# Performance work log

Measured on AMD Instinct MI355X. Metric: run time of the kernel, lower is better.

Reference implementation:

```python
import jax, jax.numpy as jnp
import numpy as np

D = 1024        # input_dim
H = 4096        # hidden_dim (expert FFN width)
RH = H // 2     # router hidden
E = 8           # expert_count
TOP_K = 2
N = 4096        # tokens
LN_EPS = 1e-5


def setup_inputs() -> dict:
    key = jax.random.key(0)
    ks = jax.random.split(key, 12)
    s_d = 1.0 / np.sqrt(D)
    s_h = 1.0 / np.sqrt(H)
    s_rh = 1.0 / np.sqrt(RH)
    return {
        "x": jax.random.normal(ks[0], (N, D), jnp.float32),
        "ln_g": jnp.ones((D,), jnp.float32),
        "ln_b": jnp.zeros((D,), jnp.float32),
        # router: Linear(D, RH) -> ReLU -> Linear(RH, E)
        "rw1": jax.random.uniform(ks[1], (D, RH), jnp.float32, -s_d, s_d),
        "rb1": jax.random.uniform(ks[2], (RH,), jnp.float32, -s_d, s_d),
        "rw2": jax.random.uniform(ks[3], (RH, E), jnp.float32, -s_rh, s_rh),
        "rb2": jax.random.uniform(ks[4], (E,), jnp.float32, -s_rh, s_rh),
        # experts: E x (Linear(D, H) -> ReLU -> Linear(H, D)); dropout is identity in eval
        "ew1": jax.random.uniform(ks[5], (E, D, H), jnp.float32, -s_d, s_d),
        "eb1": jax.random.uniform(ks[6], (E, H), jnp.float32, -s_d, s_d),
        "ew2": jax.random.uniform(ks[7], (E, H, D), jnp.float32, -s_h, s_h),
        "eb2": jax.random.uniform(ks[8], (E, D), jnp.float32, -s_h, s_h),
    }


def reference(x, ln_g, ln_b, rw1, rb1, rw2, rb2, ew1, eb1, ew2, eb2):
    residual = x
    # LayerNorm
    mu = jnp.mean(x, axis=-1, keepdims=True)
    var = jnp.mean(jnp.square(x - mu), axis=-1, keepdims=True)
    xn = (x - mu) * jax.lax.rsqrt(var + LN_EPS) * ln_g + ln_b
    # Router MLP + softmax + top-k with renormalized gates
    logits = jax.nn.relu(xn @ rw1 + rb1) @ rw2 + rb2          # [N, E]
    probs = jax.nn.softmax(logits, axis=-1)
    vals, idx = jax.lax.top_k(probs, TOP_K)                    # [N, K]
    vals = vals / jnp.sum(vals, axis=-1, keepdims=True)
    # combine weights per expert: [N, E]
    combine = jnp.sum(jax.nn.one_hot(idx, E, dtype=vals.dtype) * vals[..., None], axis=1)
    # dense grouped expert FFN: h [E, N, H], y [E, N, D]
    h = jax.nn.relu(jnp.einsum("nd,edh->enh", xn, ew1) + eb1[:, None, :])
    y = jnp.einsum("enh,ehd->end", h, ew2) + eb2[:, None, :]
    out = residual + jnp.einsum("end,ne->nd", y, combine)
    return out
```

## Files before the change

### kernel.cpp

```cpp
#include <hip/hip_runtime.h>
#include <stdint.h>

#define D_    1024
#define H_    4096
#define RH_   2048
#define E_    8
#define N_    4096
#define NK_   8192
#define MT_MAX 71
#define DELTA_MARGIN 1e-4f
#define FIX_CAP 256

typedef __bf16 bf16x8 __attribute__((ext_vector_type(8)));
typedef float  f32x4  __attribute__((ext_vector_type(4)));


__device__ __forceinline__ unsigned short f2bf(float f) {
  union { float f; unsigned u; } v; v.f = f;
  unsigned r = v.u + 0x7fffu + ((v.u >> 16) & 1u);
  return (unsigned short)(r >> 16);
}
__device__ __forceinline__ float bf2f(unsigned short h) {
  union { unsigned u; float f; } v; v.u = ((unsigned)h) << 16;
  return v.f;
}

#define GLOAD16(gp, lp) \
  __builtin_amdgcn_global_load_lds((__attribute__((address_space(1))) void*)(void*)(gp), \
                                   (__attribute__((address_space(3))) void*)(lp), 16, 0, 0)

__global__ __launch_bounds__(256) void k_transpose(const float* __restrict__ in,
                                                   unsigned short* __restrict__ outH,
                                                   unsigned short* __restrict__ outL,
                                                   int R, int C) {
  __shared__ float t[32][33];
  const int b = blockIdx.z;
  const int c0 = blockIdx.x * 32, r0 = blockIdx.y * 32;
  const int lx = threadIdx.x & 31, ly = threadIdx.x >> 5;
  const long inB = (long)R * C;
  #pragma unroll
  for (int i = 0; i < 4; i++) {
    int r = r0 + ly + i * 8;
    t[ly + i * 8][lx] = in[b * inB + (long)r * C + c0 + lx];
  }
  __syncthreads();
  #pragma unroll
  for (int i = 0; i < 4; i++) {
    int c = c0 + ly + i * 8;
    float v = t[lx][ly + i * 8];
    unsigned short h = f2bf(v);
    long oi = b * inB + (long)c * R + r0 + lx;
    outH[oi] = h;
    if (outL) outL[oi] = f2bf(v - bf2f(h));
  }
}

__global__ __launch_bounds__(256) void k_layernorm(const float* __restrict__ x,
                                                   const float* __restrict__ g,
                                                   const float* __restrict__ b,
                                                   unsigned short* __restrict__ xnh,
                                                   unsigned short* __restrict__ xnl) {
  __shared__ float red[4];
  const int n = blockIdx.x, tid = threadIdx.x;
  float4 v = ((const float4*)(x + (long)n * D_))[tid];
  float s = v.x + v.y + v.z + v.w;
  #pragma unroll
  for (int o = 32; o >= 1; o >>= 1) s += __shfl_xor(s, o, 64);
  if ((tid & 63) == 0) red[tid >> 6] = s;
  __syncthreads();
  float mean = (red[0] + red[1] + red[2] + red[3]) * (1.f / D_);
  __syncthreads();
  float d0 = v.x - mean, d1 = v.y - mean, d2 = v.z - mean, d3 = v.w - mean;
  float ss = d0 * d0 + d1 * d1 + d2 * d2 + d3 * d3;
  #pragma unroll
  for (int o = 32; o >= 1; o >>= 1) ss += __shfl_xor(ss, o, 64);
  if ((tid & 63) == 0) red[tid >> 6] = ss;
  __syncthreads();
  float rstd = rsqrtf((red[0] + red[1] + red[2] + red[3]) * (1.f / D_) + 1e-5f);
  float4 gg = ((const float4*)g)[tid];
  float4 bb = ((const float4*)b)[tid];
  float xn0 = d0 * rstd * gg.x + bb.x;
  float xn1 = d1 * rstd * gg.y + bb.y;
  float xn2 = d2 * rstd * gg.z + bb.z;
  float xn3 = d3 * rstd * gg.w + bb.w;
  unsigned short h0 = f2bf(xn0), h1 = f2bf(xn1), h2 = f2bf(xn2), h3 = f2bf(xn3);
  ((ushort4*)xnh)[(long)n * 256 + tid] = make_ushort4(h0, h1, h2, h3);
  ((ushort4*)xnl)[(long)n * 256 + tid] = make_ushort4(
      f2bf(xn0 - bf2f(h0)), f2bf(xn1 - bf2f(h1)),
      f2bf(xn2 - bf2f(h2)), f2bf(xn3 - bf2f(h3)));
}

__global__ void k_init(int* ctl) { if (threadIdx.x < 36) ctl[threadIdx.x] = 0; }

__global__ __launch_bounds__(256) void k_router_gemm(const unsigned short* __restrict__ xh,
                                                     const unsigned short* __restrict__ xl,
                                                     const unsigned short* __restrict__ bhT,
                                                     const unsigned short* __restrict__ blT,
                                                     const float* __restrict__ rb1,
                                                     float* __restrict__ h_r) {
  __shared__ __align__(16) unsigned short Ah[128 * 32], Al[128 * 32], Bh[128 * 32], Bl[128 * 32];
  const int tid = threadIdx.x, lane = tid & 63, wid = tid >> 6;
  const int m0 = blockIdx.x * 128, n0 = blockIdx.y * 128;
  const int wm = wid >> 1, wn = wid & 1;
  const int seg0 = wid * 2;
  const int srow = lane >> 2;
  const int scol = (lane & 3) * 8;
  const long a0 = (long)(m0 + seg0 * 16 + srow) * D_ + scol;
  const long a1 = a0 + 16 * D_;
  const long b0 = (long)(n0 + seg0 * 16 + srow) * D_ + scol;
  const long b1 = b0 + 16 * D_;
  const int rl = lane & 15, kh8 = (lane >> 4) * 8;
  f32x4 acc[4][4];
  #pragma unroll
  for (int i = 0; i < 4; i++)
    #pragma unroll
    for (int j = 0; j < 4; j++) acc[i][j] = 0.f;

  for (int k0 = 0; k0 < D_; k0 += 32) {
    GLOAD16(xh + a0 + k0, Ah + seg0 * 512);
    GLOAD16(xh + a1 + k0, Ah + seg0 * 512 + 512);
    GLOAD16(xl + a0 + k0, Al + seg0 * 512);
    GLOAD16(xl + a1 + k0, Al + seg0 * 512 + 512);
    GLOAD16(bhT + b0 + k0, Bh + seg0 * 512);
    GLOAD16(bhT + b1 + k0, Bh + seg0 * 512 + 512);
    GLOAD16(blT + b0 + k0, Bl + seg0 * 512);
    GLOAD16(blT + b1 + k0, Bl + seg0 * 512 + 512);
    __syncthreads();
    bf16x8 bhf[4], blf[4];
    #pragma unroll
    for (int ni = 0; ni < 4; ni++) {
      int r = (wn * 64 + ni * 16 + rl) * 32 + kh8;
      bhf[ni] = *(const bf16x8*)(Bh + r);
      blf[ni] = *(const bf16x8*)(Bl + r);
    }
    #pragma unroll
    for (int mi = 0; mi < 4; mi++) {
      int r = (wm * 64 + mi * 16 + rl) * 32 + kh8;
      bf16x8 ah = *(const bf16x8*)(Ah + r);
      bf16x8 al = *(const bf16x8*)(Al + r);
      #pragma unroll
      for (int ni = 0; ni < 4; ni++) {
        acc[mi][ni] = __builtin_amdgcn_mfma_f32_16x16x32_bf16(ah, bhf[ni], acc[mi][ni], 0, 0, 0);
        acc[mi][ni] = __builtin_amdgcn_mfma_f32_16x16x32_bf16(ah, blf[ni], acc[mi][ni], 0, 0, 0);
        acc[mi][ni] = __builtin_amdgcn_mfma_f32_16x16x32_bf16(al, bhf[ni], acc[mi][ni], 0, 0, 0);
      }
    }
    __syncthreads();
  }
  const int rg4 = (lane >> 4) * 4;
  #pragma unroll
  for (int ni = 0; ni < 4; ni++) {
    int col = n0 + wn * 64 + ni * 16 + rl;
    float bias = rb1[col];
    #pragma unroll
    for (int mi = 0; mi < 4; mi++) {
      int row = m0 + wm * 64 + mi * 16 + rg4;
      #pragma unroll
      for (int r = 0; r < 4; r++) {
        float v = acc[mi][ni][r] + bias;
        h_r[(long)(row + r) * RH_ + col] = v > 0.f ? v : 0.f;
      }
    }
  }
}

__global__ __launch_bounds__(256) void k_logits_top2(const float* __restrict__ h_r,
                                                     const float* __restrict__ rw2,
                                                     const float* __restrict__ rb2,
                                                     int* __restrict__ sel, float* __restrict__ gate,
                                                     int* __restrict__ marked, int* __restrict__ mcount) {
  const int lane = threadIdx.x & 63, wid = threadIdx.x >> 6;
  const int n = blockIdx.x * 4 + wid;
  float p[8] = {0, 0, 0, 0, 0, 0, 0, 0};
  const float* hr = h_r + (long)n * RH_;
  for (int i = 0; i < RH_ / 64; i++) {
    int c = i * 64 + lane;
    float v = hr[c];
    float4 wa = ((const float4*)(rw2 + c * 8))[0];
    float4 wb = ((const float4*)(rw2 + c * 8))[1];
    p[0] += v * wa.x; p[1] += v * wa.y; p[2] += v * wa.z; p[3] += v * wa.w;
    p[4] += v * wb.x; p[5] += v * wb.y; p[6] += v * wb.z; p[7] += v * wb.w;
  }
  #pragma unroll
  for (int e = 0; e < 8; e++)
    #pragma unroll
    for (int s = 32; s >= 1; s >>= 1) p[e] += __shfl_xor(p[e], s, 64);
  if (lane == 0) {
    float l1 = -1e30f, l2 = -1e30f, l3 = -1e30f; int e1 = 0, e2 = 0;
    #pragma unroll
    for (int e = 0; e < 8; e++) {
      float v = p[e] + rb2[e];
      if (v > l1)      { l3 = l2; l2 = l1; e2 = e1; l1 = v; e1 = e; }
      else if (v > l2) { l3 = l2; l2 = v; e2 = e; }
      else if (v > l3) { l3 = v; }
    }
    float g1 = 1.f / (1.f + expf(l2 - l1));
    sel[n * 2] = e1; sel[n * 2 + 1] = e2;
    gate[n * 2] = g1; gate[n * 2 + 1] = 1.f - g1;
    if (l2 - l3 < DELTA_MARGIN) { int i = atomicAdd(mcount, 1); marked[i] = n; }
  }
}

__global__ __launch_bounds__(256) void k_fixup1(const float* __restrict__ x,
                                                const float* __restrict__ ln_g, const float* __restrict__ ln_b,
                                                const float* __restrict__ rw1, const float* __restrict__ rb1,
                                                const int* __restrict__ marked, const int* __restrict__ mcount,
                                                double* __restrict__ hsbuf) {
  __shared__ float xs[D_];
  __shared__ float redf[4];
  __shared__ double part[64][5];
  const int tid = threadIdx.x;
  int cnt = *mcount; if (cnt > FIX_CAP) cnt = FIX_CAP;
  const int blkTok = blockIdx.x >> 5;
  const int chunk  = blockIdx.x & 31;
  for (int mi = blkTok; mi < cnt; mi += FIX_CAP) {
    const int n = marked[mi];
    float4 v = ((const float4*)(x + (long)n * D_))[tid];
    float s = v.x + v.y + v.z + v.w;
    #pragma unroll
    for (int o = 32; o >= 1; o >>= 1) s += __shfl_xor(s, o, 64);
    if ((tid & 63) == 0) redf[tid >> 6] = s;
    __syncthreads();
    float mean = (redf[0] + redf[1] + redf[2] + redf[3]) * (1.f / D_);
    __syncthreads();
    float d0 = v.x - mean, d1 = v.y - mean, d2 = v.z - mean, d3 = v.w - mean;
    float ss = d0 * d0 + d1 * d1 + d2 * d2 + d3 * d3;
    #pragma unroll
    for (int o = 32; o >= 1; o >>= 1) ss += __shfl_xor(ss, o, 64);
    if ((tid & 63) == 0) redf[tid >> 6] = ss;
    __syncthreads();
    float rstd = rsqrtf((redf[0] + redf[1] + redf[2] + redf[3]) * (1.f / D_) + 1e-5f);
    float4 gg = ((const float4*)ln_g)[tid];
    float4 bb = ((const float4*)ln_b)[tid];
    xs[tid * 4 + 0] = d0 * rstd * gg.x + bb.x;
    xs[tid * 4 + 1] = d1 * rstd * gg.y + bb.y;
    xs[tid * 4 + 2] = d2 * rstd * gg.z + bb.z;
    xs[tid * 4 + 3] = d3 * rstd * gg.w + bb.w;
    __syncthreads();
    const int lcol = tid & 63, prt = tid >> 6;
    const int col = chunk * 64 + lcol;
    const float* rp = rw1 + (long)(prt * 256) * RH_ + col;
    const float* xp = xs + prt * 256;
    double a0 = 0, a1 = 0, a2 = 0, a3 = 0;
    #pragma unroll 4
    for (int d = 0; d < 256; d += 4) {
      float w0 = rp[(long)(d + 0) * RH_];
      float w1 = rp[(long)(d + 1) * RH_];
      float w2 = rp[(long)(d + 2) * RH_];
      float w3 = rp[(long)(d + 3) * RH_];
      a0 += (double)xp[d + 0] * (double)w0;
      a1 += (double)xp[d + 1] * (double)w1;
      a2 += (double)xp[d + 2] * (double)w2;
      a3 += (double)xp[d + 3] * (double)w3;
    }
    part[lcol][prt] = (a0 + a1) + (a2 + a3);
    __syncthreads();
    if (tid < 64) {
      double a = (part[tid][0] + part[tid][1]) + (part[tid][2] + part[tid][3])
               + (double)rb1[chunk * 64 + tid];
      hsbuf[(long)mi * RH_ + chunk * 64 + tid] = a > 0.0 ? a : 0.0;
    }
    __syncthreads();
  }
}

__global__ __launch_bounds__(256) void k_fixup2(const double* __restrict__ hsbuf,
                                                const float* __restrict__ rw2, const float* __restrict__ rb2,
                                                const int* __restrict__ marked, const int* __restrict__ mcount,
                                                int* __restrict__ sel, float* __restrict__ gate) {
  __shared__ double red2[256];
  const int tid = threadIdx.x;
  int cnt = *mcount; if (cnt > FIX_CAP) cnt = FIX_CAP;
  for (int mi = blockIdx.x; mi < cnt; mi += gridDim.x) {
    const int n = marked[mi];
    const double* hs = hsbuf + (long)mi * RH_;
    const int e = tid & 7, ch = tid >> 3;
    double pp = 0.0;
    for (int c = ch * 64; c < ch * 64 + 64; c++) pp += hs[c] * (double)rw2[c * 8 + e];
    red2[tid] = pp;
    __syncthreads();
    if (tid < 128) red2[tid] += red2[tid + 128];
    __syncthreads();
    if (tid < 64) red2[tid] += red2[tid + 64];
    __syncthreads();
    if (tid < 32) red2[tid] += red2[tid + 32];
    __syncthreads();
    if (tid < 16) red2[tid] += red2[tid + 16];
    __syncthreads();
    if (tid < 8) red2[tid] += red2[tid + 8];
    __syncthreads();
    if (tid == 0) {
      double l1 = -1e300, l2 = -1e300; int e1 = 0, e2 = 0;
      for (int ee = 0; ee < 8; ee++) {
        double vv = red2[ee] + (double)rb2[ee];
        if (vv > l1)      { l2 = l1; e2 = e1; l1 = vv; e1 = ee; }
        else if (vv > l2) { l2 = vv; e2 = ee; }
      }
      double g1 = 1.0 / (1.0 + exp(l2 - l1));
      sel[n * 2] = e1; sel[n * 2 + 1] = e2;
      gate[n * 2] = (float)g1; gate[n * 2 + 1] = (float)(1.0 - g1);
    }
    __syncthreads();
  }
}

__global__ void k_count(const int* __restrict__ sel, int* ctl) {
  int n = blockIdx.x * 256 + threadIdx.x;
  if (n >= N_) return;
  atomicAdd(&ctl[sel[n * 2]], 1);
  atomicAdd(&ctl[sel[n * 2 + 1]], 1);
}
__global__ void k_offsets(int* ctl) {
  if (threadIdx.x == 0 && blockIdx.x == 0) {
    int t = 0, tt = 0;
    for (int e = 0; e < 8; e++) {
      ctl[8 + e] = t; ctl[17 + e] = tt; ctl[26 + e] = t;
      t += ctl[e]; tt += (ctl[e] + 127) >> 7;
    }
    ctl[16] = t; ctl[25] = tt;
  }
}
__global__ void k_scatter(const int* __restrict__ sel, int* ctl,
                          int* __restrict__ perm, int* __restrict__ pos) {
  int n = blockIdx.x * 256 + threadIdx.x;
  if (n >= N_) return;
  #pragma unroll
  for (int k = 0; k < 2; k++) {
    int e = sel[n * 2 + k];
    int p = atomicAdd(&ctl[26 + e], 1);
    perm[p] = n;
    pos[n * 2 + k] = p;
  }
}

template <int KD, bool GATHER, bool RELU_BF16>
__global__ __launch_bounds__(256) void k_gemm_expert(const unsigned short* __restrict__ A,
                                                     const unsigned short* __restrict__ BT,
                                                     const float* __restrict__ bias,
                                                     const int* __restrict__ ctl,
                                                     const int* __restrict__ perm,
                                                     unsigned short* __restrict__ outBF,
                                                     float* __restrict__ outF32, int NB) {
  const int* cnt = ctl; const int* off = ctl + 8; const int* toff = ctl + 17;
  const int mt = blockIdx.y;
  if (mt >= toff[8]) return;
  int e = 0;
  #pragma unroll
  for (int i = 0; i < 7; i++) if (toff[i + 1] <= mt) e = i + 1;
  const int ltile = mt - toff[e];
  const int g0 = off[e] + ltile * 128;
  int vrows = cnt[e] - ltile * 128; if (vrows > 128) vrows = 128;
  const int n0 = blockIdx.x * 128;

  __shared__ __align__(16) unsigned short At[128 * 32], Bt[128 * 32];
  __shared__ int pidx[128];
  const int tid = threadIdx.x, lane = tid & 63, wid = tid >> 6;
  if constexpr (GATHER) {
    if (tid < 128) {
      int g = g0 + tid, gmax = off[e] + cnt[e] - 1;
      pidx[tid] = perm[g <= gmax ? g : gmax];
    }
    __syncthreads();
  }
  const int seg0 = wid * 2;
  const int srow0 = seg0 * 16 + (lane >> 2);
  const int scol = (lane & 3) * 8;
  long ab0, ab1;
  if constexpr (GATHER) {
    ab0 = (long)pidx[srow0] * KD + scol;
    ab1 = (long)pidx[srow0 + 16] * KD + scol;
  } else {
    ab0 = (long)(g0 + srow0) * KD + scol;
    ab1 = ab0 + (long)16 * KD;
  }
  const long bbase = (long)e * NB * KD;
  const long bb0 = bbase + (long)(n0 + srow0) * KD + scol;
  const long bb1 = bb0 + (long)16 * KD;

  const int wm = wid >> 1, wn = wid & 1;
  const int rl = lane & 15, kh8 = (lane >> 4) * 8;
  f32x4 acc[4][4];
  #pragma unroll
  for (int i = 0; i < 4; i++)
    #pragma unroll
    for (int j = 0; j < 4; j++) acc[i][j] = 0.f;

  for (int k0 = 0; k0 < KD; k0 += 32) {
    GLOAD16(A + ab0 + k0, At + seg0 * 512);
    GLOAD16(A + ab1 + k0, At + seg0 * 512 + 512);
    GLOAD16(BT + bb0 + k0, Bt + seg0 * 512);
    GLOAD16(BT + bb1 + k0, Bt + seg0 * 512 + 512);
    __syncthreads();
    bf16x8 bfr[4];
    #pragma unroll
    for (int ni = 0; ni < 4; ni++)
      bfr[ni] = *(const bf16x8*)(Bt + (wn * 64 + ni * 16 + rl) * 32 + kh8);
    #pragma unroll
    for (int mi = 0; mi < 4; mi++) {
      bf16x8 af = *(const bf16x8*)(At + (wm * 64 + mi * 16 + rl) * 32 + kh8);
      #pragma unroll
      for (int ni = 0; ni < 4; ni++)
        acc[mi][ni] = __builtin_amdgcn_mfma_f32_16x16x32_bf16(af, bfr[ni], acc[mi][ni], 0, 0, 0);
    }
    __syncthreads();
  }
  const int rg4 = (lane >> 4) * 4;
  #pragma unroll
  for (int ni = 0; ni < 4; ni++) {
    int col = n0 + wn * 64 + ni * 16 + rl;
    float bv = bias[(long)e * NB + col];
    #pragma unroll
    for (int mi = 0; mi < 4; mi++) {
      int lrow = wm * 64 + mi * 16 + rg4;
      #pragma unroll
      for (int r = 0; r < 4; r++) {
        if (lrow + r < vrows) {
          float v = acc[mi][ni][r] + bv;
          long idx = (long)(g0 + lrow + r) * NB + col;
          if constexpr (RELU_BF16) outBF[idx] = f2bf(v > 0.f ? v : 0.f);
          else outF32[idx] = v;
        }
      }
    }
  }
}

__global__ __launch_bounds__(256) void k_combine(const float* __restrict__ x,
                                                 const float* __restrict__ y_buf,
                                                 const int* __restrict__ pos,
                                                 const float* __restrict__ gate,
                                                 float* __restrict__ out) {
  const int n = blockIdx.x, t = threadIdx.x;
  const float g0 = gate[n * 2], g1 = gate[n * 2 + 1];
  const long p0 = pos[n * 2], p1 = pos[n * 2 + 1];
  float4 xv = ((const float4*)(x + (long)n * D_))[t];
  float4 a = ((const float4*)(y_buf + p0 * D_))[t];
  float4 b = ((const float4*)(y_buf + p1 * D_))[t];
  float4 o;
  o.x = xv.x + g0 * a.x + g1 * b.x;
  o.y = xv.y + g0 * a.y + g1 * b.y;
  o.z = xv.z + g0 * a.z + g1 * b.z;
  o.w = xv.w + g0 * a.w + g1 * b.w;
  ((float4*)(out + (long)n * D_))[t] = o;
}

extern "C" void kernel_launch(void* const* d_in, const int* in_sizes, int n_in,
                              void* d_out, int out_size, void* d_ws, size_t ws_size,
                              hipStream_t stream) {
  const float* x    = (const float*)d_in[0];
  const float* ln_g = (const float*)d_in[1];
  const float* ln_b = (const float*)d_in[2];
  const float* rw1  = (const float*)d_in[3];
  const float* rb1  = (const float*)d_in[4];
  const float* rw2  = (const float*)d_in[5];
  const float* rb2  = (const float*)d_in[6];
  const float* ew1  = (const float*)d_in[7];
  const float* eb1  = (const float*)d_in[8];
  const float* ew2  = (const float*)d_in[9];
  const float* eb2  = (const float*)d_in[10];
  float* out = (float*)d_out;

  char* w = (char*)d_ws;
  size_t off = 0;
  auto alloc = [&](size_t bytes) -> char* {
    char* p = w + off;
    off += (bytes + 255) & ~(size_t)255;
    return p;
  };
  unsigned short* ew1T  = (unsigned short*)alloc((size_t)E_ * H_ * D_ * 2);
  unsigned short* ew2T  = (unsigned short*)alloc((size_t)E_ * D_ * H_ * 2);
  unsigned short* rw1hT = (unsigned short*)alloc((size_t)RH_ * D_ * 2);
  unsigned short* rw1lT = (unsigned short*)alloc((size_t)RH_ * D_ * 2);
  unsigned short* xnh   = (unsigned short*)alloc((size_t)N_ * D_ * 2);
  unsigned short* xnl   = (unsigned short*)alloc((size_t)N_ * D_ * 2);
  float*          h_r   = (float*)alloc((size_t)N_ * RH_ * 4);
  unsigned short* h_buf = (unsigned short*)alloc((size_t)(NK_ + 128) * H_ * 2);
  float*          y_buf = (float*)alloc((size_t)(NK_ + 128) * D_ * 4);
  double*         hsbuf = (double*)alloc((size_t)FIX_CAP * RH_ * 8);
  int*   sel    = (int*)alloc((size_t)N_ * 2 * 4);
  float* gate   = (float*)alloc((size_t)N_ * 2 * 4);
  int*   marked = (int*)alloc((size_t)N_ * 4);
  int*   perm   = (int*)alloc((size_t)NK_ * 4);
  int*   pos    = (int*)alloc((size_t)N_ * 2 * 4);
  int*   ctl    = (int*)alloc(64 * 4);

  k_transpose<<<dim3(H_ / 32, D_ / 32, E_), 256, 0, stream>>>(ew1, ew1T, nullptr, D_, H_);
  k_transpose<<<dim3(D_ / 32, H_ / 32, E_), 256, 0, stream>>>(ew2, ew2T, nullptr, H_, D_);
  k_transpose<<<dim3(RH_ / 32, D_ / 32, 1), 256, 0, stream>>>(rw1, rw1hT, rw1lT, D_, RH_);
  k_layernorm<<<N_, 256, 0, stream>>>(x, ln_g, ln_b, xnh, xnl);
  k_init<<<1, 64, 0, stream>>>(ctl);
  k_router_gemm<<<dim3(N_ / 128, RH_ / 128), 256, 0, stream>>>(xnh, xnl, rw1hT, rw1lT, rb1, h_r);
  k_logits_top2<<<N_ / 4, 256, 0, stream>>>(h_r, rw2, rb2, sel, gate, marked, ctl + 34);
  k_fixup1<<<FIX_CAP * 32, 256, 0, stream>>>(x, ln_g, ln_b, rw1, rb1, marked, ctl + 34, hsbuf);
  k_fixup2<<<64, 256, 0, stream>>>(hsbuf, rw2, rb2, marked, ctl + 34, sel, gate);
  k_count<<<N_ / 256, 256, 0, stream>>>(sel, ctl);
  k_offsets<<<1, 1, 0, stream>>>(ctl);
  k_scatter<<<N_ / 256, 256, 0, stream>>>(sel, ctl, perm, pos);
  k_gemm_expert<D_, true, true><<<dim3(H_ / 128, MT_MAX), 256, 0, stream>>>(
      xnh, ew1T, eb1, ctl, perm, h_buf, nullptr, H_);
  k_gemm_expert<H_, false, false><<<dim3(D_ / 128, MT_MAX), 256, 0, stream>>>(
      h_buf, ew2T, eb2, ctl, perm, nullptr, y_buf, D_);
  k_combine<<<N_, 256, 0, stream>>>(x, y_buf, pos, gate, out);

  (void)in_sizes; (void)n_in; (void)out_size; (void)ws_size;
}
```

Before: 546.7 us.

## Enlarge expert GEMM tiles to 256 rows with 512-thread blocks and XCD-aware remap

The expert GEMMs now use 256-row M tiles, with 256x256 tiles for the first GEMM and 256x128 for the second, run by 512-thread workgroups. Tile offsets are recomputed per expert in 256-row granularity. The workgroup index is remapped so that consecutive tiles land on the same XCD, which should improve L2 reuse of weight and activation tiles. Larger tiles raise arithmetic intensity and cut redundant global loads, at the cost of more padding waste per expert, higher register pressure (an 8x4 accumulator array per wave in the first GEMM), and fewer workgroups to fill the GPU.

```diff
diff --git a/kernel.cpp b/kernel.cpp
--- a/kernel.cpp
+++ b/kernel.cpp
@@ -7,7 +7,7 @@
 #define E_    8
 #define N_    4096
 #define NK_   8192
-#define MT_MAX 71
+#define MT256_MAX 39
 #define DELTA_MARGIN 1e-4f
 #define FIX_CAP 256
 
@@ -90,7 +90,7 @@
       f2bf(xn2 - bf2f(h2)), f2bf(xn3 - bf2f(h3)));
 }
 
-__global__ void k_init(int* ctl) { if (threadIdx.x < 36) ctl[threadIdx.x] = 0; }
+__global__ void k_init(int* ctl) { if (threadIdx.x < 46) ctl[threadIdx.x] = 0; }
 
 __global__ __launch_bounds__(256) void k_router_gemm(const unsigned short* __restrict__ xh,
                                                      const unsigned short* __restrict__ xl,
@@ -312,12 +312,12 @@
 }
 __global__ void k_offsets(int* ctl) {
   if (threadIdx.x == 0 && blockIdx.x == 0) {
-    int t = 0, tt = 0;
+    int t = 0, t2 = 0;
     for (int e = 0; e < 8; e++) {
-      ctl[8 + e] = t; ctl[17 + e] = tt; ctl[26 + e] = t;
-      t += ctl[e]; tt += (ctl[e] + 127) >> 7;
-    }
-    ctl[16] = t; ctl[25] = tt;
+      ctl[8 + e] = t; ctl[26 + e] = t; ctl[36 + e] = t2;
+      t += ctl[e]; t2 += (ctl[e] + 255) >> 8;
+    }
+    ctl[16] = t; ctl[44] = t2;
   }
 }
 __global__ void k_scatter(const int* __restrict__ sel, int* ctl,
@@ -333,71 +333,93 @@
   }
 }
 
-template <int KD, bool GATHER, bool RELU_BF16>
-__global__ __launch_bounds__(256) void k_gemm_expert(const unsigned short* __restrict__ A,
-                                                     const unsigned short* __restrict__ BT,
-                                                     const float* __restrict__ bias,
-                                                     const int* __restrict__ ctl,
-                                                     const int* __restrict__ perm,
-                                                     unsigned short* __restrict__ outBF,
-                                                     float* __restrict__ outF32, int NB) {
-  const int* cnt = ctl; const int* off = ctl + 8; const int* toff = ctl + 17;
-  const int mt = blockIdx.y;
+template <int KD, int BN, bool GATHER, bool RELU_BF16, bool MTFAST>
+__global__ __launch_bounds__(512, 2) void k_gemm_expert2(const unsigned short* __restrict__ A,
+                                                         const unsigned short* __restrict__ BT,
+                                                         const float* __restrict__ bias,
+                                                         const int* __restrict__ ctl,
+                                                         const int* __restrict__ perm,
+                                                         unsigned short* __restrict__ outBF,
+                                                         float* __restrict__ outF32, int NB) {
+  const int* cnt = ctl; const int* off = ctl + 8; const int* toff = ctl + 36;
+  const int NX = gridDim.x, MT = gridDim.y;
+  const int nwg = NX * MT;
+  const int F = blockIdx.y * NX + blockIdx.x;
+  const int q = nwg >> 3, r8 = nwg & 7;
+  const int xcd = F & 7, j = F >> 3;
+  const int L = (xcd < r8 ? xcd * (q + 1) : r8 * (q + 1) + (xcd - r8) * q) + j;
+  int mt, nt;
+  if (MTFAST) { mt = L % MT; nt = L / MT; }
+  else        { nt = L % NX; mt = L / NX; }
   if (mt >= toff[8]) return;
   int e = 0;
   #pragma unroll
   for (int i = 0; i < 7; i++) if (toff[i + 1] <= mt) e = i + 1;
   const int ltile = mt - toff[e];
-  const int g0 = off[e] + ltile * 128;
-  int vrows = cnt[e] - ltile * 128; if (vrows > 128) vrows = 128;
-  const int n0 = blockIdx.x * 128;
-
-  __shared__ __align__(16) unsigned short At[128 * 32], Bt[128 * 32];
-  __shared__ int pidx[128];
+  const int g0 = off[e] + ltile * 256;
+  int vrows = cnt[e] - ltile * 256; if (vrows > 256) vrows = 256;
+  const int n0 = nt * BN;
+
+  __shared__ __align__(16) unsigned short At[256 * 32], Bt[BN * 32];
+  __shared__ int pidx[256];
   const int tid = threadIdx.x, lane = tid & 63, wid = tid >> 6;
   if constexpr (GATHER) {
-    if (tid < 128) {
+    if (tid < 256) {
       int g = g0 + tid, gmax = off[e] + cnt[e] - 1;
       pidx[tid] = perm[g <= gmax ? g : gmax];
     }
     __syncthreads();
   }
-  const int seg0 = wid * 2;
-  const int srow0 = seg0 * 16 + (lane >> 2);
+  const int srow = lane >> 2;
   const int scol = (lane & 3) * 8;
-  long ab0, ab1;
+  const int arow0 = wid * 32 + srow;
+  const int arow1 = arow0 + 16;
+  long aa0, aa1;
   if constexpr (GATHER) {
-    ab0 = (long)pidx[srow0] * KD + scol;
-    ab1 = (long)pidx[srow0 + 16] * KD + scol;
+    aa0 = (long)pidx[arow0] * KD + scol;
+    aa1 = (long)pidx[arow1] * KD + scol;
   } else {
-    ab0 = (long)(g0 + srow0) * KD + scol;
-    ab1 = ab0 + (long)16 * KD;
+    aa0 = (long)(g0 + arow0) * KD + scol;
+    aa1 = aa0 + (long)16 * KD;
   }
   const long bbase = (long)e * NB * KD;
-  const long bb0 = bbase + (long)(n0 + srow0) * KD + scol;
-  const long bb1 = bb0 + (long)16 * KD;
-
-  const int wm = wid >> 1, wn = wid & 1;
+  long ba0, ba1;
+  if constexpr (BN == 256) {
+    ba0 = bbase + (long)(n0 + wid * 32 + srow) * KD + scol;
+    ba1 = ba0 + (long)16 * KD;
+  } else {
+    ba0 = bbase + (long)(n0 + wid * 16 + srow) * KD + scol;
+    ba1 = 0;
+  }
+
+  constexpr int WN = BN / 64;
+  constexpr int MR = (BN == 256) ? 8 : 4;
+  constexpr int WROW = (BN == 256) ? 128 : 64;
+  const int wm = wid / WN, wn = wid % WN;
   const int rl = lane & 15, kh8 = (lane >> 4) * 8;
-  f32x4 acc[4][4];
-  #pragma unroll
-  for (int i = 0; i < 4; i++)
-    #pragma unroll
-    for (int j = 0; j < 4; j++) acc[i][j] = 0.f;
+  f32x4 acc[MR][4];
+  #pragma unroll
+  for (int i = 0; i < MR; i++)
+    #pragma unroll
+    for (int jj = 0; jj < 4; jj++) acc[i][jj] = 0.f;
 
   for (int k0 = 0; k0 < KD; k0 += 32) {
-    GLOAD16(A + ab0 + k0, At + seg0 * 512);
-    GLOAD16(A + ab1 + k0, At + seg0 * 512 + 512);
-    GLOAD16(BT + bb0 + k0, Bt + seg0 * 512);
-    GLOAD16(BT + bb1 + k0, Bt + seg0 * 512 + 512);
+    GLOAD16(A + aa0 + k0, At + (wid * 2) * 512);
+    GLOAD16(A + aa1 + k0, At + (wid * 2) * 512 + 512);
+    if constexpr (BN == 256) {
+      GLOAD16(BT + ba0 + k0, Bt + (wid * 2) * 512);
+      GLOAD16(BT + ba1 + k0, Bt + (wid * 2) * 512 + 512);
+    } else {
+      GLOAD16(BT + ba0 + k0, Bt + wid * 512);
+    }
     __syncthreads();
     bf16x8 bfr[4];
     #pragma unroll
     for (int ni = 0; ni < 4; ni++)
       bfr[ni] = *(const bf16x8*)(Bt + (wn * 64 + ni * 16 + rl) * 32 + kh8);
     #pragma unroll
-    for (int mi = 0; mi < 4; mi++) {
-      bf16x8 af = *(const bf16x8*)(At + (wm * 64 + mi * 16 + rl) * 32 + kh8);
+    for (int mi = 0; mi < MR; mi++) {
+      bf16x8 af = *(const bf16x8*)(At + (wm * WROW + mi * 16 + rl) * 32 + kh8);
       #pragma unroll
       for (int ni = 0; ni < 4; ni++)
         acc[mi][ni] = __builtin_amdgcn_mfma_f32_16x16x32_bf16(af, bfr[ni], acc[mi][ni], 0, 0, 0);
@@ -410,8 +432,8 @@
     int col = n0 + wn * 64 + ni * 16 + rl;
     float bv = bias[(long)e * NB + col];
     #pragma unroll
-    for (int mi = 0; mi < 4; mi++) {
-      int lrow = wm * 64 + mi * 16 + rg4;
+    for (int mi = 0; mi < MR; mi++) {
+      int lrow = wm * WROW + mi * 16 + rg4;
       #pragma unroll
       for (int r = 0; r < 4; r++) {
         if (lrow + r < vrows) {
@@ -474,8 +496,8 @@
   unsigned short* xnh   = (unsigned short*)alloc((size_t)N_ * D_ * 2);
   unsigned short* xnl   = (unsigned short*)alloc((size_t)N_ * D_ * 2);
   float*          h_r   = (float*)alloc((size_t)N_ * RH_ * 4);
-  unsigned short* h_buf = (unsigned short*)alloc((size_t)(NK_ + 128) * H_ * 2);
-  float*          y_buf = (float*)alloc((size_t)(NK_ + 128) * D_ * 4);
+  unsigned short* h_buf = (unsigned short*)alloc((size_t)(NK_ + 256) * H_ * 2);
+  float*          y_buf = (float*)alloc((size_t)(NK_ + 256) * D_ * 4);
   double*         hsbuf = (double*)alloc((size_t)FIX_CAP * RH_ * 8);
   int*   sel    = (int*)alloc((size_t)N_ * 2 * 4);
   float* gate   = (float*)alloc((size_t)N_ * 2 * 4);
@@ -496,9 +518,9 @@
   k_count<<<N_ / 256, 256, 0, stream>>>(sel, ctl);
   k_offsets<<<1, 1, 0, stream>>>(ctl);
   k_scatter<<<N_ / 256, 256, 0, stream>>>(sel, ctl, perm, pos);
-  k_gemm_expert<D_, true, true><<<dim3(H_ / 128, MT_MAX), 256, 0, stream>>>(
+  k_gemm_expert2<D_, 256, true, true, true><<<dim3(H_ / 256, MT256_MAX), 512, 0, stream>>>(
       xnh, ew1T, eb1, ctl, perm, h_buf, nullptr, H_);
-  k_gemm_expert<H_, false, false><<<dim3(D_ / 128, MT_MAX), 256, 0, stream>>>(
+  k_gemm_expert2<H_, 128, false, false, false><<<dim3(D_ / 128, MT256_MAX), 512, 0, stream>>>(
       h_buf, ew2T, eb2, ctl, perm, nullptr, y_buf, D_);
   k_combine<<<N_, 256, 0, stream>>>(x, y_buf, pos, gate, out);
 
```

After: 599.7 us. +9.7%, slower.
